# Optimization experiments

Hardware: AMD Instinct MI355X
Metric: run time of the kernel (lower is better)

Reference implementation:

```python
import jax, jax.numpy as jnp
import numpy as np

B, S = 512, 64
ZD, GD, SK = 256, 16, 512   # vel_z_dim, genre_cond_dim, skel_encode_dim
H = 1024                    # vel_hidden_dim
ND, VC = 9, 4               # n_drum_classes, vel_cond_dim


def _gru(x, h, Wi, Wh, bi, bh):
    # torch.nn.GRUCell math; gates ordered [r, z, n]
    gi = x @ Wi.T + bi
    gh = h @ Wh.T + bh
    i_r, i_z, i_n = jnp.split(gi, 3, axis=-1)
    h_r, h_z, h_n = jnp.split(gh, 3, axis=-1)
    r = jax.nn.sigmoid(i_r + h_r)
    zg = jax.nn.sigmoid(i_z + h_z)
    n = jnp.tanh(i_n + r * h_n)
    return (1.0 - zg) * n + zg * h


def setup_inputs() -> dict:
    key = jax.random.key(0)
    ks = jax.random.split(key, 14)
    rn = lambda k, shp, s: jax.random.normal(k, shp, dtype=jnp.float32) * s
    return dict(
        z=rn(ks[0], (B, ZD), 1.0),
        note_encoded=rn(ks[1], (B, SK), 1.0),
        vel_target=jax.random.uniform(ks[2], (B, S, ND), dtype=jnp.float32),
        note=jax.random.uniform(ks[3], (B, S, ND), dtype=jnp.float32),
        vel_cond=jax.random.uniform(ks[4], (B, S, VC), dtype=jnp.float32),
        genre_cond=rn(ks[5], (B, GD), 1.0),
        W_in=rn(ks[6], (H, ZD + SK + GD), 0.02), b_in=jnp.zeros((H,), jnp.float32),
        W_ih1=rn(ks[7], (3 * H, ND * 2 + VC), 0.05), W_hh1=rn(ks[8], (3 * H, H), 0.02),
        b_ih1=jnp.zeros((3 * H,), jnp.float32), b_hh1=jnp.zeros((3 * H,), jnp.float32),
        W_ih2=rn(ks[9], (3 * H, H), 0.02), W_hh2=rn(ks[10], (3 * H, H), 0.02),
        b_ih2=jnp.zeros((3 * H,), jnp.float32), b_hh2=jnp.zeros((3 * H,), jnp.float32),
        W_out=rn(ks[11], (ND, H), 0.02), b_out=jnp.zeros((ND,), jnp.float32),
        training=0, teacher_forcing_ratio=0,
    )


def reference(z, note_encoded, vel_target, note, vel_cond, genre_cond,
              W_in, b_in, W_ih1, W_hh1, b_ih1, b_hh1,
              W_ih2, W_hh2, b_ih2, b_hh2, W_out, b_out,
              training, teacher_forcing_ratio):
    # eval mode: dropout = identity, teacher forcing never taken
    del vel_target, training, teacher_forcing_ratio
    bsz = z.shape[0]
    zc = jnp.concatenate([z.reshape(bsz, -1), note_encoded, genre_cond], axis=-1)
    h1 = jnp.tanh(zc @ W_in.T + b_in)              # [B, H]
    h2 = jnp.zeros_like(h1)                        # overwritten at step 0
    out0 = jnp.zeros((bsz, W_out.shape[0]), z.dtype)

    def step(carry, xs):
        out, h1, h2 = carry
        i, nt, ct = xs
        inp = jnp.concatenate([out, nt, ct], axis=-1)       # [B, 2*ND+VC]
        h1 = _gru(inp, h1, W_ih1, W_hh1, b_ih1, b_hh1)
        h2 = jnp.where(i == 0, h1, h2)                      # hx[1] = hx[0] at i==0
        h2 = _gru(h1, h2, W_ih2, W_hh2, b_ih2, b_hh2)
        vel = jax.nn.sigmoid(h2 @ W_out.T + b_out)          # [B, ND]
        return (vel, h1, h2), vel

    xs = (jnp.arange(note.shape[1]),
          jnp.transpose(note, (1, 0, 2)),
          jnp.transpose(vel_cond, (1, 0, 2)))
    _, outs = jax.lax.scan(step, (out0, h1, h2), xs)
    return jnp.transpose(outs, (1, 0, 2))                    # [B, S, ND]
```

## Files before the change

### kernel.cpp

```cpp
#include <hip/hip_runtime.h>
#include <hip/hip_bf16.h>

#define HD 1024
#define BB 512
#define SS 64
#define N3 3072
#define NC 9216
#define ND 9
#define VC 4

typedef __attribute__((ext_vector_type(8))) short bf16x8;
typedef __attribute__((ext_vector_type(4))) float f32x4;

__device__ __forceinline__ ushort f2b(float f) {
    unsigned u = __builtin_bit_cast(unsigned, f);
    u += 0x7fffu + ((u >> 16) & 1u);
    return (ushort)(u >> 16);
}

__device__ __forceinline__ void gld_lds16(const void* g, void* l) {
    __builtin_amdgcn_global_load_lds(
        (const __attribute__((address_space(1))) unsigned int*)g,
        (__attribute__((address_space(3))) unsigned int*)l, 16, 0, 0);
}

__global__ __launch_bounds__(256) void prep_w(
    const float* __restrict__ Wih2, const float* __restrict__ Whh1,
    const float* __restrict__ Whh2, ushort* __restrict__ Wcat)
{
    const int row = blockIdx.x;
    const float* src = row < 3072 ? Wih2 + (size_t)row * HD
                     : row < 6144 ? Whh1 + (size_t)(row - 3072) * HD
                                  : Whh2 + (size_t)(row - 6144) * HD;
    const int c = threadIdx.x * 4;
    float4 v = *(const float4*)(src + c);
    ushort4 o;
    o.x = f2b(v.x); o.y = f2b(v.y); o.z = f2b(v.z); o.w = f2b(v.w);
    *(ushort4*)(Wcat + (size_t)row * HD + c) = o;
}

__global__ __launch_bounds__(256) void prep_wt1(
    const float* __restrict__ Wih1, float* __restrict__ Wt1)
{
    const int g = blockIdx.x * 256 + threadIdx.x;
    #pragma unroll
    for (int c = 0; c < 22; ++c)
        Wt1[c * N3 + g] = Wih1[(size_t)g * 22 + c];
}

__global__ __launch_bounds__(256) void init_h1(
    const float* __restrict__ z, const float* __restrict__ ne, const float* __restrict__ gc,
    const float* __restrict__ W_in, const float* __restrict__ b_in,
    float* __restrict__ h1, ushort* __restrict__ h1b)
{
    __shared__ float As[16][68];
    __shared__ float Ws[16][68];

    const int tid = threadIdx.x;
    const int bm  = blockIdx.y * 64;
    const int bn  = blockIdx.x * 64;
    const int r   = tid >> 2;
    const int kq  = (tid & 3) << 2;
    const int ty  = tid >> 4;
    const int tx  = tid & 15;
    const int brow = bm + r;

    float acc[4][4] = {};

    for (int k0 = 0; k0 < 784; k0 += 16) {
        const int c = k0 + kq;
        float4 a;
        if (c < 256)      a = *(const float4*)(z  + (size_t)brow * 256 + c);
        else if (c < 768) a = *(const float4*)(ne + (size_t)brow * 512 + (c - 256));
        else              a = *(const float4*)(gc + (size_t)brow * 16  + (c - 768));
        float4 w = *(const float4*)(W_in + (size_t)(bn + r) * 784 + c);
        __syncthreads();
        As[kq+0][r] = a.x; As[kq+1][r] = a.y; As[kq+2][r] = a.z; As[kq+3][r] = a.w;
        Ws[kq+0][r] = w.x; Ws[kq+1][r] = w.y; Ws[kq+2][r] = w.z; Ws[kq+3][r] = w.w;
        __syncthreads();
        #pragma unroll
        for (int k = 0; k < 16; ++k) {
            float4 avv = *(const float4*)&As[k][ty * 4];
            float4 wvv = *(const float4*)&Ws[k][tx * 4];
            const float av[4] = {avv.x, avv.y, avv.z, avv.w};
            const float wv[4] = {wvv.x, wvv.y, wvv.z, wvv.w};
            #pragma unroll
            for (int i = 0; i < 4; ++i)
                #pragma unroll
                for (int j = 0; j < 4; ++j)
                    acc[i][j] = fmaf(av[i], wv[j], acc[i][j]);
        }
    }
    const int col = bn + tx * 4;
    float4 bi = *(const float4*)(b_in + col);
    const float bv[4] = {bi.x, bi.y, bi.z, bi.w};
    #pragma unroll
    for (int i = 0; i < 4; ++i) {
        const int row = bm + ty * 4 + i;
        float4 o = make_float4(tanhf(acc[i][0] + bv[0]), tanhf(acc[i][1] + bv[1]),
                               tanhf(acc[i][2] + bv[2]), tanhf(acc[i][3] + bv[3]));
        *(float4*)(h1 + (size_t)row * HD + col) = o;
        ushort4 ob; ob.x = f2b(o.x); ob.y = f2b(o.y); ob.z = f2b(o.z); ob.w = f2b(o.w);
        *(ushort4*)(h1b + (size_t)row * HD + col) = ob;
    }
}

__global__ __launch_bounds__(256) void gemm3(
    const ushort* __restrict__ h1b, const ushort* __restrict__ h2b,
    const ushort* __restrict__ Wcat, float* __restrict__ Cbuf, int ntb)
{
    __shared__ __align__(16) ushort As[4096];
    __shared__ __align__(16) ushort Ws[4096];

    const int flat = blockIdx.x + (blockIdx.y << 3);
    const int id   = (flat & 7) * gridDim.y + (flat >> 3);
    const int bm   = (id & 7) << 6;
    const int nt   = (id >> 3) + ntb;

    const ushort* Amat = (nt < 96) ? h1b : h2b;
    const ushort* W    = Wcat + (size_t)(nt << 6) * HD;

    const int tid = threadIdx.x;
    const int w   = tid >> 6;
    const int l   = tid & 63;

    const int srow = l >> 3;
    const int sch  = ((l & 7) ^ srow) << 3;
    const ushort* Ag0 = Amat + (size_t)(bm + 16 * w + srow) * HD + sch;
    const ushort* Ag1 = Ag0 + 8 * HD;
    const ushort* Wg0 = W + (size_t)(16 * w + srow) * HD + sch;
    const ushort* Wg1 = Wg0 + 8 * HD;
    ushort* Al0 = As + (16 * w) * 64;
    ushort* Al1 = As + (16 * w + 8) * 64;
    ushort* Wl0 = Ws + (16 * w) * 64;
    ushort* Wl1 = Ws + (16 * w + 8) * 64;

    const int wm = (w >> 1) << 5;
    const int wn = (w & 1) << 5;
    const int fr = l & 15;
    const int fc = l >> 4;

    const int ra0 = wm + fr,  ra1 = wm + 16 + fr;
    const int rb0 = wn + fr,  rb1 = wn + 16 + fr;

    f32x4 acc00 = {0.f,0.f,0.f,0.f}, acc01 = {0.f,0.f,0.f,0.f};
    f32x4 acc10 = {0.f,0.f,0.f,0.f}, acc11 = {0.f,0.f,0.f,0.f};

    for (int kt = 0; kt < 16; ++kt) {
        const int ko = kt << 6;
        __syncthreads();
        gld_lds16(Ag0 + ko, Al0);
        gld_lds16(Ag1 + ko, Al1);
        gld_lds16(Wg0 + ko, Wl0);
        gld_lds16(Wg1 + ko, Wl1);
        __syncthreads();
        #pragma unroll
        for (int kk = 0; kk < 2; ++kk) {
            const int c = (kk << 2) + fc;
            bf16x8 a0 = *(const bf16x8*)(As + ra0 * 64 + ((c ^ (ra0 & 7)) << 3));
            bf16x8 a1 = *(const bf16x8*)(As + ra1 * 64 + ((c ^ (ra1 & 7)) << 3));
            bf16x8 b0 = *(const bf16x8*)(Ws + rb0 * 64 + ((c ^ (rb0 & 7)) << 3));
            bf16x8 b1 = *(const bf16x8*)(Ws + rb1 * 64 + ((c ^ (rb1 & 7)) << 3));
            acc00 = __builtin_amdgcn_mfma_f32_16x16x32_bf16(a0, b0, acc00, 0, 0, 0);
            acc01 = __builtin_amdgcn_mfma_f32_16x16x32_bf16(a0, b1, acc01, 0, 0, 0);
            acc10 = __builtin_amdgcn_mfma_f32_16x16x32_bf16(a1, b0, acc10, 0, 0, 0);
            acc11 = __builtin_amdgcn_mfma_f32_16x16x32_bf16(a1, b1, acc11, 0, 0, 0);
        }
    }

    const int bn = nt << 6;
    float* Cw = Cbuf + (size_t)(bm + wm) * NC + bn + wn;
    #pragma unroll
    for (int r = 0; r < 4; ++r) {
        const size_t ro0 = (size_t)(fc * 4 + r) * NC;
        const size_t ro1 = (size_t)(16 + fc * 4 + r) * NC;
        Cw[ro0 + fr]      = acc00[r];
        Cw[ro0 + 16 + fr] = acc01[r];
        Cw[ro1 + fr]      = acc10[r];
        Cw[ro1 + 16 + fr] = acc11[r];
    }
}

__global__ __launch_bounds__(1024) void gru1_f(
    const float* __restrict__ Cbuf, float* __restrict__ h1, ushort* __restrict__ h1b,
    float* __restrict__ h2, ushort* __restrict__ h2b,
    const float* __restrict__ note, const float* __restrict__ velc,
    const float* __restrict__ dout,
    const float* __restrict__ Wt1, const float* __restrict__ b_ih1,
    const float* __restrict__ b_hh1, int step)
{
    __shared__ float inp[22];
    const int b = blockIdx.x;
    const int j = threadIdx.x;

    if (j < 22) {
        float v;
        if (j < 9)       v = (step == 0) ? 0.f : dout[(size_t)b * (SS * ND) + (step - 1) * ND + j];
        else if (j < 18) v = note[(size_t)b * (SS * ND) + step * ND + (j - 9)];
        else             v = velc[(size_t)b * (SS * VC) + step * VC + (j - 18)];
        inp[j] = v;
    }
    __syncthreads();

    float ir = b_ih1[j], iz = b_ih1[HD + j], inn = b_ih1[2 * HD + j];
    #pragma unroll
    for (int c = 0; c < 22; ++c) {
        const float x = inp[c];
        const float* wr = Wt1 + c * N3;
        ir  = fmaf(x, wr[j],          ir);
        iz  = fmaf(x, wr[HD + j],     iz);
        inn = fmaf(x, wr[2 * HD + j], inn);
    }

    const float* g = Cbuf + (size_t)b * NC + N3;
    const float hr = g[j]          + b_hh1[j];
    const float hz = g[HD + j]     + b_hh1[HD + j];
    const float hn = g[2 * HD + j] + b_hh1[2 * HD + j];

    const float rg = 1.f / (1.f + __expf(-(ir + hr)));
    const float zg = 1.f / (1.f + __expf(-(iz + hz)));
    const float n  = tanhf(inn + rg * hn);
    const float hnew = (1.f - zg) * n + zg * h1[(size_t)b * HD + j];
    h1[(size_t)b * HD + j]  = hnew;
    const ushort hb = f2b(hnew);
    h1b[(size_t)b * HD + j] = hb;
    if (step == 0) {
        h2[(size_t)b * HD + j]  = hnew;
        h2b[(size_t)b * HD + j] = hb;
    }
}

__global__ __launch_bounds__(1024) void gru2_out(
    const float* __restrict__ Cbuf, float* __restrict__ h2, ushort* __restrict__ h2b,
    const float* __restrict__ b_ih2, const float* __restrict__ b_hh2,
    const float* __restrict__ W_out, const float* __restrict__ b_out,
    float* __restrict__ dout, int step)
{
    __shared__ float hs[HD];
    const int b = blockIdx.x;
    const int j = threadIdx.x;

    const float* gi = Cbuf + (size_t)b * NC;
    const float* gh = Cbuf + (size_t)b * NC + 2 * N3;

    const float ir  = gi[j]          + b_ih2[j];
    const float hr  = gh[j]          + b_hh2[j];
    const float iz  = gi[HD + j]     + b_ih2[HD + j];
    const float hz  = gh[HD + j]     + b_hh2[HD + j];
    const float inn = gi[2 * HD + j] + b_ih2[2 * HD + j];
    const float hn  = gh[2 * HD + j] + b_hh2[2 * HD + j];

    const float rg = 1.f / (1.f + __expf(-(ir + hr)));
    const float zg = 1.f / (1.f + __expf(-(iz + hz)));
    const float n  = tanhf(inn + rg * hn);
    const float hnew = (1.f - zg) * n + zg * h2[(size_t)b * HD + j];
    h2[(size_t)b * HD + j]  = hnew;
    h2b[(size_t)b * HD + j] = f2b(hnew);
    hs[j] = hnew;
    __syncthreads();

    const int w = j >> 6;
    const int t = j & 63;
    if (w < ND) {
        float a = 0.f;
        const float* wr = W_out + (size_t)w * HD;
        #pragma unroll
        for (int k = 0; k < HD / 64; ++k)
            a = fmaf(hs[t + k * 64], wr[t + k * 64], a);
        #pragma unroll
        for (int off = 32; off > 0; off >>= 1) a += __shfl_down(a, off);
        if (t == 0)
            dout[(size_t)b * (SS * ND) + step * ND + w] =
                1.f / (1.f + __expf(-(a + b_out[w])));
    }
}

extern "C" void kernel_launch(void* const* d_in, const int* in_sizes, int n_in,
                              void* d_out, int out_size, void* d_ws, size_t ws_size,
                              hipStream_t stream)
{
    const float* z     = (const float*)d_in[0];
    const float* ne    = (const float*)d_in[1];
    const float* note  = (const float*)d_in[3];
    const float* velc  = (const float*)d_in[4];
    const float* gc    = (const float*)d_in[5];
    const float* W_in  = (const float*)d_in[6];
    const float* b_in  = (const float*)d_in[7];
    const float* W_ih1 = (const float*)d_in[8];
    const float* W_hh1 = (const float*)d_in[9];
    const float* b_ih1 = (const float*)d_in[10];
    const float* b_hh1 = (const float*)d_in[11];
    const float* W_ih2 = (const float*)d_in[12];
    const float* W_hh2 = (const float*)d_in[13];
    const float* b_ih2 = (const float*)d_in[14];
    const float* b_hh2 = (const float*)d_in[15];
    const float* W_out = (const float*)d_in[16];
    const float* b_out = (const float*)d_in[17];
    float* out = (float*)d_out;

    float* h1   = (float*)d_ws;
    float* h2   = h1 + BB * HD;
    float* Cbuf = h2 + BB * HD;
    float* Wt1  = Cbuf + (size_t)BB * NC;
    ushort* h1b = (ushort*)(Wt1 + 22 * N3);
    ushort* h2b = h1b + BB * HD;
    ushort* Wcat = h2b + BB * HD;

    prep_w <<<dim3(NC), 256, 0, stream>>>(W_ih2, W_hh1, W_hh2, Wcat);
    prep_wt1<<<dim3(12), 256, 0, stream>>>(W_ih1, Wt1);
    init_h1<<<dim3(16, 8), 256, 0, stream>>>(z, ne, gc, W_in, b_in, h1, h1b);

    gemm3<<<dim3(8, 48), 256, 0, stream>>>(h1b, h2b, Wcat, Cbuf, 48);

    for (int s = 0; s < SS; ++s) {
        gru1_f<<<dim3(BB), 1024, 0, stream>>>(Cbuf, h1, h1b, h2, h2b,
                                              note, velc, out, Wt1, b_ih1, b_hh1, s);
        gemm3<<<dim3(8, 144), 256, 0, stream>>>(h1b, h2b, Wcat, Cbuf, 0);
        gru2_out<<<dim3(BB), 1024, 0, stream>>>(Cbuf, h2, h2b, b_ih2, b_hh2,
                                                W_out, b_out, out, s);
    }
}
```

Before: 2.150 ms.

## Fuse GRU pointwise stages across steps, widen GEMM tile, MFMA init GEMM

Reschedules the recurrence so each step runs one GEMM and one fused pointwise kernel. The fused kernel computes the layer-2 GRU update and the output projection, then the next step's layer-1 GRU update, using the W_hh1·h1 product already held in Cbuf. This removes one launch per step and a round-trip of h1. The shared GEMM now uses 64x128 tiles with 8 MFMAs per k-slice for more reuse, at the cost of fewer blocks. The initial tanh(W_in·zc) becomes a bf16 MFMA GEMM over padded inputs instead of an fp32 SIMT GEMM, which lowers precision for that layer.

```diff
diff --git a/kernel.cpp b/kernel.cpp
--- a/kernel.cpp
+++ b/kernel.cpp
@@ -8,6 +8,7 @@
 #define NC 9216
 #define ND 9
 #define VC 4
+#define KI 832
 
 typedef __attribute__((ext_vector_type(8))) short bf16x8;
 typedef __attribute__((ext_vector_type(4))) float f32x4;
@@ -48,156 +49,235 @@
         Wt1[c * N3 + g] = Wih1[(size_t)g * 22 + c];
 }
 
-__global__ __launch_bounds__(256) void init_h1(
-    const float* __restrict__ z, const float* __restrict__ ne, const float* __restrict__ gc,
-    const float* __restrict__ W_in, const float* __restrict__ b_in,
-    float* __restrict__ h1, ushort* __restrict__ h1b)
-{
-    __shared__ float As[16][68];
-    __shared__ float Ws[16][68];
-
-    const int tid = threadIdx.x;
-    const int bm  = blockIdx.y * 64;
-    const int bn  = blockIdx.x * 64;
-    const int r   = tid >> 2;
-    const int kq  = (tid & 3) << 2;
-    const int ty  = tid >> 4;
-    const int tx  = tid & 15;
-    const int brow = bm + r;
-
-    float acc[4][4] = {};
-
-    for (int k0 = 0; k0 < 784; k0 += 16) {
-        const int c = k0 + kq;
-        float4 a;
-        if (c < 256)      a = *(const float4*)(z  + (size_t)brow * 256 + c);
-        else if (c < 768) a = *(const float4*)(ne + (size_t)brow * 512 + (c - 256));
-        else              a = *(const float4*)(gc + (size_t)brow * 16  + (c - 768));
-        float4 w = *(const float4*)(W_in + (size_t)(bn + r) * 784 + c);
-        __syncthreads();
-        As[kq+0][r] = a.x; As[kq+1][r] = a.y; As[kq+2][r] = a.z; As[kq+3][r] = a.w;
-        Ws[kq+0][r] = w.x; Ws[kq+1][r] = w.y; Ws[kq+2][r] = w.z; Ws[kq+3][r] = w.w;
-        __syncthreads();
-        #pragma unroll
-        for (int k = 0; k < 16; ++k) {
-            float4 avv = *(const float4*)&As[k][ty * 4];
-            float4 wvv = *(const float4*)&Ws[k][tx * 4];
-            const float av[4] = {avv.x, avv.y, avv.z, avv.w};
-            const float wv[4] = {wvv.x, wvv.y, wvv.z, wvv.w};
-            #pragma unroll
-            for (int i = 0; i < 4; ++i)
-                #pragma unroll
-                for (int j = 0; j < 4; ++j)
-                    acc[i][j] = fmaf(av[i], wv[j], acc[i][j]);
-        }
-    }
-    const int col = bn + tx * 4;
-    float4 bi = *(const float4*)(b_in + col);
-    const float bv[4] = {bi.x, bi.y, bi.z, bi.w};
-    #pragma unroll
-    for (int i = 0; i < 4; ++i) {
-        const int row = bm + ty * 4 + i;
-        float4 o = make_float4(tanhf(acc[i][0] + bv[0]), tanhf(acc[i][1] + bv[1]),
-                               tanhf(acc[i][2] + bv[2]), tanhf(acc[i][3] + bv[3]));
-        *(float4*)(h1 + (size_t)row * HD + col) = o;
-        ushort4 ob; ob.x = f2b(o.x); ob.y = f2b(o.y); ob.z = f2b(o.z); ob.w = f2b(o.w);
-        *(ushort4*)(h1b + (size_t)row * HD + col) = ob;
-    }
+__global__ __launch_bounds__(256) void prep_acat(
+    const float* __restrict__ z, const float* __restrict__ ne,
+    const float* __restrict__ gc, ushort* __restrict__ Acat)
+{
+    const int b = blockIdx.x;
+    const int t = threadIdx.x;
+    if (t >= 208) return;
+    const int c = t * 4;
+    float4 v = make_float4(0.f, 0.f, 0.f, 0.f);
+    if (c < 256)      v = *(const float4*)(z  + (size_t)b * 256 + c);
+    else if (c < 768) v = *(const float4*)(ne + (size_t)b * 512 + (c - 256));
+    else if (c < 784) v = *(const float4*)(gc + (size_t)b * 16  + (c - 768));
+    ushort4 o;
+    o.x = f2b(v.x); o.y = f2b(v.y); o.z = f2b(v.z); o.w = f2b(v.w);
+    *(ushort4*)(Acat + (size_t)b * KI + c) = o;
+}
+
+__global__ __launch_bounds__(256) void prep_win(
+    const float* __restrict__ W_in, ushort* __restrict__ W_inb)
+{
+    const int r = blockIdx.x;
+    const int t = threadIdx.x;
+    if (t >= 208) return;
+    const int c = t * 4;
+    ushort4 o = {0, 0, 0, 0};
+    if (c < 784) {
+        float4 v = *(const float4*)(W_in + (size_t)r * 784 + c);
+        o.x = f2b(v.x); o.y = f2b(v.y); o.z = f2b(v.z); o.w = f2b(v.w);
+    }
+    *(ushort4*)(W_inb + (size_t)r * KI + c) = o;
 }
 
 __global__ __launch_bounds__(256) void gemm3(
     const ushort* __restrict__ h1b, const ushort* __restrict__ h2b,
     const ushort* __restrict__ Wcat, float* __restrict__ Cbuf, int ntb)
 {
-    __shared__ __align__(16) ushort As[4096];
-    __shared__ __align__(16) ushort Ws[4096];
+    __shared__ __align__(16) ushort As[64 * 64];
+    __shared__ __align__(16) ushort Bs[128 * 64];
 
     const int flat = blockIdx.x + (blockIdx.y << 3);
     const int id   = (flat & 7) * gridDim.y + (flat >> 3);
-    const int bm   = (id & 7) << 6;
-    const int nt   = (id >> 3) + ntb;
-
-    const ushort* Amat = (nt < 96) ? h1b : h2b;
-    const ushort* W    = Wcat + (size_t)(nt << 6) * HD;
+    const int mt   = id & 7;
+    const int n2   = (id >> 3) + ntb;
+    const int bm   = mt << 6;
+
+    const ushort* Amat = (n2 < 48) ? h1b : h2b;
+    const ushort* Wb   = Wcat + (size_t)(n2 << 7) * HD;
 
     const int tid = threadIdx.x;
     const int w   = tid >> 6;
     const int l   = tid & 63;
-
-    const int srow = l >> 3;
-    const int sch  = ((l & 7) ^ srow) << 3;
-    const ushort* Ag0 = Amat + (size_t)(bm + 16 * w + srow) * HD + sch;
+    const int lr  = l >> 3;
+    const int sw  = ((l & 7) ^ lr) << 3;
+
+    const ushort* Ag0 = Amat + (size_t)(bm + 16 * w + lr) * HD + sw;
     const ushort* Ag1 = Ag0 + 8 * HD;
-    const ushort* Wg0 = W + (size_t)(16 * w + srow) * HD + sch;
-    const ushort* Wg1 = Wg0 + 8 * HD;
+    const ushort* Bg0 = Wb + (size_t)(32 * w + lr) * HD + sw;
+    const ushort* Bg1 = Bg0 + 8 * HD;
+    const ushort* Bg2 = Bg0 + 16 * HD;
+    const ushort* Bg3 = Bg0 + 24 * HD;
     ushort* Al0 = As + (16 * w) * 64;
     ushort* Al1 = As + (16 * w + 8) * 64;
-    ushort* Wl0 = Ws + (16 * w) * 64;
-    ushort* Wl1 = Ws + (16 * w + 8) * 64;
-
-    const int wm = (w >> 1) << 5;
-    const int wn = (w & 1) << 5;
-    const int fr = l & 15;
-    const int fc = l >> 4;
-
-    const int ra0 = wm + fr,  ra1 = wm + 16 + fr;
-    const int rb0 = wn + fr,  rb1 = wn + 16 + fr;
-
-    f32x4 acc00 = {0.f,0.f,0.f,0.f}, acc01 = {0.f,0.f,0.f,0.f};
-    f32x4 acc10 = {0.f,0.f,0.f,0.f}, acc11 = {0.f,0.f,0.f,0.f};
+    ushort* Bl0 = Bs + (32 * w) * 64;
+    ushort* Bl1 = Bs + (32 * w + 8) * 64;
+    ushort* Bl2 = Bs + (32 * w + 16) * 64;
+    ushort* Bl3 = Bs + (32 * w + 24) * 64;
+
+    const int wm2 = w >> 1;
+    const int wn2 = w & 1;
+    const int fr  = l & 15;
+    const int fc  = l >> 4;
+
+    f32x4 acc[2][4] = {};
 
     for (int kt = 0; kt < 16; ++kt) {
         const int ko = kt << 6;
         __syncthreads();
         gld_lds16(Ag0 + ko, Al0);
         gld_lds16(Ag1 + ko, Al1);
-        gld_lds16(Wg0 + ko, Wl0);
-        gld_lds16(Wg1 + ko, Wl1);
+        gld_lds16(Bg0 + ko, Bl0);
+        gld_lds16(Bg1 + ko, Bl1);
+        gld_lds16(Bg2 + ko, Bl2);
+        gld_lds16(Bg3 + ko, Bl3);
         __syncthreads();
         #pragma unroll
         for (int kk = 0; kk < 2; ++kk) {
             const int c = (kk << 2) + fc;
-            bf16x8 a0 = *(const bf16x8*)(As + ra0 * 64 + ((c ^ (ra0 & 7)) << 3));
-            bf16x8 a1 = *(const bf16x8*)(As + ra1 * 64 + ((c ^ (ra1 & 7)) << 3));
-            bf16x8 b0 = *(const bf16x8*)(Ws + rb0 * 64 + ((c ^ (rb0 & 7)) << 3));
-            bf16x8 b1 = *(const bf16x8*)(Ws + rb1 * 64 + ((c ^ (rb1 & 7)) << 3));
-            acc00 = __builtin_amdgcn_mfma_f32_16x16x32_bf16(a0, b0, acc00, 0, 0, 0);
-            acc01 = __builtin_amdgcn_mfma_f32_16x16x32_bf16(a0, b1, acc01, 0, 0, 0);
-            acc10 = __builtin_amdgcn_mfma_f32_16x16x32_bf16(a1, b0, acc10, 0, 0, 0);
-            acc11 = __builtin_amdgcn_mfma_f32_16x16x32_bf16(a1, b1, acc11, 0, 0, 0);
-        }
-    }
-
-    const int bn = nt << 6;
-    float* Cw = Cbuf + (size_t)(bm + wm) * NC + bn + wn;
+            bf16x8 a[2], b[4];
+            #pragma unroll
+            for (int i = 0; i < 2; ++i) {
+                const int ra = (wm2 << 5) + (i << 4) + fr;
+                a[i] = *(const bf16x8*)(As + ra * 64 + ((c ^ (ra & 7)) << 3));
+            }
+            #pragma unroll
+            for (int j = 0; j < 4; ++j) {
+                const int rb = (wn2 << 6) + (j << 4) + fr;
+                b[j] = *(const bf16x8*)(Bs + rb * 64 + ((c ^ (rb & 7)) << 3));
+            }
+            #pragma unroll
+            for (int i = 0; i < 2; ++i)
+                #pragma unroll
+                for (int j = 0; j < 4; ++j)
+                    acc[i][j] = __builtin_amdgcn_mfma_f32_16x16x32_bf16(a[i], b[j], acc[i][j], 0, 0, 0);
+        }
+    }
+
+    const int bn = n2 << 7;
     #pragma unroll
-    for (int r = 0; r < 4; ++r) {
-        const size_t ro0 = (size_t)(fc * 4 + r) * NC;
-        const size_t ro1 = (size_t)(16 + fc * 4 + r) * NC;
-        Cw[ro0 + fr]      = acc00[r];
-        Cw[ro0 + 16 + fr] = acc01[r];
-        Cw[ro1 + fr]      = acc10[r];
-        Cw[ro1 + 16 + fr] = acc11[r];
-    }
-}
-
-__global__ __launch_bounds__(1024) void gru1_f(
+    for (int i = 0; i < 2; ++i) {
+        const int row0 = bm + (wm2 << 5) + (i << 4) + (fc << 2);
+        #pragma unroll
+        for (int r = 0; r < 4; ++r) {
+            float* Crow = Cbuf + (size_t)(row0 + r) * NC + bn + (wn2 << 6) + fr;
+            Crow[0]  = acc[i][0][r];
+            Crow[16] = acc[i][1][r];
+            Crow[32] = acc[i][2][r];
+            Crow[48] = acc[i][3][r];
+        }
+    }
+}
+
+__global__ __launch_bounds__(256) void gemm_init(
+    const ushort* __restrict__ Acat, const ushort* __restrict__ W_inb,
+    const float* __restrict__ b_in, float* __restrict__ h1, ushort* __restrict__ h1b)
+{
+    __shared__ __align__(16) ushort As[64 * 64];
+    __shared__ __align__(16) ushort Bs[128 * 64];
+
+    const int flat = blockIdx.x + (blockIdx.y << 3);
+    const int id   = (flat & 7) * gridDim.y + (flat >> 3);
+    const int mt   = id & 7;
+    const int n2   = id >> 3;
+    const int bm   = mt << 6;
+
+    const ushort* Wb = W_inb + (size_t)(n2 << 7) * KI;
+
+    const int tid = threadIdx.x;
+    const int w   = tid >> 6;
+    const int l   = tid & 63;
+    const int lr  = l >> 3;
+    const int sw  = ((l & 7) ^ lr) << 3;
+
+    const ushort* Ag0 = Acat + (size_t)(bm + 16 * w + lr) * KI + sw;
+    const ushort* Ag1 = Ag0 + 8 * KI;
+    const ushort* Bg0 = Wb + (size_t)(32 * w + lr) * KI + sw;
+    const ushort* Bg1 = Bg0 + 8 * KI;
+    const ushort* Bg2 = Bg0 + 16 * KI;
+    const ushort* Bg3 = Bg0 + 24 * KI;
+    ushort* Al0 = As + (16 * w) * 64;
+    ushort* Al1 = As + (16 * w + 8) * 64;
+    ushort* Bl0 = Bs + (32 * w) * 64;
+    ushort* Bl1 = Bs + (32 * w + 8) * 64;
+    ushort* Bl2 = Bs + (32 * w + 16) * 64;
+    ushort* Bl3 = Bs + (32 * w + 24) * 64;
+
+    const int wm2 = w >> 1;
+    const int wn2 = w & 1;
+    const int fr  = l & 15;
+    const int fc  = l >> 4;
+
+    f32x4 acc[2][4] = {};
+
+    for (int kt = 0; kt < 13; ++kt) {
+        const int ko = kt << 6;
+        __syncthreads();
+        gld_lds16(Ag0 + ko, Al0);
+        gld_lds16(Ag1 + ko, Al1);
+        gld_lds16(Bg0 + ko, Bl0);
+        gld_lds16(Bg1 + ko, Bl1);
+        gld_lds16(Bg2 + ko, Bl2);
+        gld_lds16(Bg3 + ko, Bl3);
+        __syncthreads();
+        #pragma unroll
+        for (int kk = 0; kk < 2; ++kk) {
+            const int c = (kk << 2) + fc;
+            bf16x8 a[2], b[4];
+            #pragma unroll
+            for (int i = 0; i < 2; ++i) {
+                const int ra = (wm2 << 5) + (i << 4) + fr;
+                a[i] = *(const bf16x8*)(As + ra * 64 + ((c ^ (ra & 7)) << 3));
+            }
+            #pragma unroll
+            for (int j = 0; j < 4; ++j) {
+                const int rb = (wn2 << 6) + (j << 4) + fr;
+                b[j] = *(const bf16x8*)(Bs + rb * 64 + ((c ^ (rb & 7)) << 3));
+            }
+            #pragma unroll
+            for (int i = 0; i < 2; ++i)
+                #pragma unroll
+                for (int j = 0; j < 4; ++j)
+                    acc[i][j] = __builtin_amdgcn_mfma_f32_16x16x32_bf16(a[i], b[j], acc[i][j], 0, 0, 0);
+        }
+    }
+
+    const int bn = (n2 << 7) + (wn2 << 6) + fr;
+    float bj[4];
+    #pragma unroll
+    for (int j = 0; j < 4; ++j) bj[j] = b_in[bn + (j << 4)];
+    #pragma unroll
+    for (int i = 0; i < 2; ++i) {
+        const int row0 = bm + (wm2 << 5) + (i << 4) + (fc << 2);
+        #pragma unroll
+        for (int r = 0; r < 4; ++r) {
+            #pragma unroll
+            for (int j = 0; j < 4; ++j) {
+                const float v = tanhf(acc[i][j][r] + bj[j]);
+                const size_t idx = (size_t)(row0 + r) * HD + bn + (j << 4);
+                h1[idx]  = v;
+                h1b[idx] = f2b(v);
+            }
+        }
+    }
+}
+
+__global__ __launch_bounds__(1024) void gru1_first(
     const float* __restrict__ Cbuf, float* __restrict__ h1, ushort* __restrict__ h1b,
     float* __restrict__ h2, ushort* __restrict__ h2b,
     const float* __restrict__ note, const float* __restrict__ velc,
-    const float* __restrict__ dout,
     const float* __restrict__ Wt1, const float* __restrict__ b_ih1,
-    const float* __restrict__ b_hh1, int step)
+    const float* __restrict__ b_hh1)
 {
     __shared__ float inp[22];
     const int b = blockIdx.x;
     const int j = threadIdx.x;
 
     if (j < 22) {
-        float v;
-        if (j < 9)       v = (step == 0) ? 0.f : dout[(size_t)b * (SS * ND) + (step - 1) * ND + j];
-        else if (j < 18) v = note[(size_t)b * (SS * ND) + step * ND + (j - 9)];
-        else             v = velc[(size_t)b * (SS * VC) + step * VC + (j - 18)];
+        float v = 0.f;
+        if (j >= 9 && j < 18) v = note[(size_t)b * (SS * ND) + (j - 9)];
+        else if (j >= 18)     v = velc[(size_t)b * (SS * VC) + (j - 18)];
         inp[j] = v;
     }
     __syncthreads();
@@ -221,27 +301,35 @@
     const float zg = 1.f / (1.f + __expf(-(iz + hz)));
     const float n  = tanhf(inn + rg * hn);
     const float hnew = (1.f - zg) * n + zg * h1[(size_t)b * HD + j];
+    const ushort hb = f2b(hnew);
     h1[(size_t)b * HD + j]  = hnew;
-    const ushort hb = f2b(hnew);
     h1b[(size_t)b * HD + j] = hb;
-    if (step == 0) {
-        h2[(size_t)b * HD + j]  = hnew;
-        h2b[(size_t)b * HD + j] = hb;
-    }
-}
-
-__global__ __launch_bounds__(1024) void gru2_out(
-    const float* __restrict__ Cbuf, float* __restrict__ h2, ushort* __restrict__ h2b,
+    h2[(size_t)b * HD + j]  = hnew;
+    h2b[(size_t)b * HD + j] = hb;
+}
+
+__global__ __launch_bounds__(1024) void pw_fused(
+    const float* __restrict__ Cbuf, float* __restrict__ h1, ushort* __restrict__ h1b,
+    float* __restrict__ h2, ushort* __restrict__ h2b,
+    const float* __restrict__ note, const float* __restrict__ velc,
+    const float* __restrict__ Wt1,
+    const float* __restrict__ b_ih1, const float* __restrict__ b_hh1,
     const float* __restrict__ b_ih2, const float* __restrict__ b_hh2,
     const float* __restrict__ W_out, const float* __restrict__ b_out,
     float* __restrict__ dout, int step)
 {
     __shared__ float hs[HD];
+    __shared__ float inp[22];
     const int b = blockIdx.x;
     const int j = threadIdx.x;
 
+    if (step + 1 < SS && j >= 9 && j < 22) {
+        inp[j] = (j < 18) ? note[(size_t)b * (SS * ND) + (step + 1) * ND + (j - 9)]
+                          : velc[(size_t)b * (SS * VC) + (step + 1) * VC + (j - 18)];
+    }
+
     const float* gi = Cbuf + (size_t)b * NC;
-    const float* gh = Cbuf + (size_t)b * NC + 2 * N3;
+    const float* gh = gi + 2 * N3;
 
     const float ir  = gi[j]          + b_ih2[j];
     const float hr  = gh[j]          + b_hh2[j];
@@ -269,9 +357,35 @@
             a = fmaf(hs[t + k * 64], wr[t + k * 64], a);
         #pragma unroll
         for (int off = 32; off > 0; off >>= 1) a += __shfl_down(a, off);
-        if (t == 0)
-            dout[(size_t)b * (SS * ND) + step * ND + w] =
-                1.f / (1.f + __expf(-(a + b_out[w])));
+        if (t == 0) {
+            const float o = 1.f / (1.f + __expf(-(a + b_out[w])));
+            dout[(size_t)b * (SS * ND) + step * ND + w] = o;
+            inp[w] = o;
+        }
+    }
+    __syncthreads();
+
+    if (step + 1 < SS) {
+        float xir = b_ih1[j], xiz = b_ih1[HD + j], xinn = b_ih1[2 * HD + j];
+        #pragma unroll
+        for (int c = 0; c < 22; ++c) {
+            const float x = inp[c];
+            const float* wr = Wt1 + c * N3;
+            xir  = fmaf(x, wr[j],          xir);
+            xiz  = fmaf(x, wr[HD + j],     xiz);
+            xinn = fmaf(x, wr[2 * HD + j], xinn);
+        }
+        const float* g1 = Cbuf + (size_t)b * NC + N3;
+        const float hr1 = g1[j]          + b_hh1[j];
+        const float hz1 = g1[HD + j]     + b_hh1[HD + j];
+        const float hn1 = g1[2 * HD + j] + b_hh1[2 * HD + j];
+
+        const float rg1 = 1.f / (1.f + __expf(-(xir + hr1)));
+        const float zg1 = 1.f / (1.f + __expf(-(xiz + hz1)));
+        const float n1  = tanhf(xinn + rg1 * hn1);
+        const float h1new = (1.f - zg1) * n1 + zg1 * h1[(size_t)b * HD + j];
+        h1[(size_t)b * HD + j]  = h1new;
+        h1b[(size_t)b * HD + j] = f2b(h1new);
     }
 }
 
@@ -298,25 +412,32 @@
     const float* b_out = (const float*)d_in[17];
     float* out = (float*)d_out;
 
-    float* h1   = (float*)d_ws;
-    float* h2   = h1 + BB * HD;
-    float* Cbuf = h2 + BB * HD;
-    float* Wt1  = Cbuf + (size_t)BB * NC;
-    ushort* h1b = (ushort*)(Wt1 + 22 * N3);
-    ushort* h2b = h1b + BB * HD;
+    float*  h1   = (float*)d_ws;
+    float*  h2   = h1 + BB * HD;
+    float*  Cbuf = h2 + BB * HD;
+    float*  Wt1  = Cbuf + (size_t)BB * NC;
+    ushort* h1b  = (ushort*)(Wt1 + 22 * N3);
+    ushort* h2b  = h1b + BB * HD;
     ushort* Wcat = h2b + BB * HD;
-
-    prep_w <<<dim3(NC), 256, 0, stream>>>(W_ih2, W_hh1, W_hh2, Wcat);
-    prep_wt1<<<dim3(12), 256, 0, stream>>>(W_ih1, Wt1);
-    init_h1<<<dim3(16, 8), 256, 0, stream>>>(z, ne, gc, W_in, b_in, h1, h1b);
-
-    gemm3<<<dim3(8, 48), 256, 0, stream>>>(h1b, h2b, Wcat, Cbuf, 48);
+    ushort* Acat  = (ushort*)Cbuf;
+    ushort* W_inb = Acat + (size_t)BB * KI;
+
+    prep_w   <<<dim3(NC),  256, 0, stream>>>(W_ih2, W_hh1, W_hh2, Wcat);
+    prep_wt1 <<<dim3(12),  256, 0, stream>>>(W_ih1, Wt1);
+    prep_acat<<<dim3(BB),  256, 0, stream>>>(z, ne, gc, Acat);
+    prep_win <<<dim3(HD),  256, 0, stream>>>(W_in, W_inb);
+
+    gemm_init<<<dim3(8, 8), 256, 0, stream>>>(Acat, W_inb, b_in, h1, h1b);
+
+    gemm3<<<dim3(8, 24), 256, 0, stream>>>(h1b, h2b, Wcat, Cbuf, 24);
+    gru1_first<<<dim3(BB), 1024, 0, stream>>>(Cbuf, h1, h1b, h2, h2b,
+                                              note, velc, Wt1, b_ih1, b_hh1);
 
     for (int s = 0; s < SS; ++s) {
-        gru1_f<<<dim3(BB), 1024, 0, stream>>>(Cbuf, h1, h1b, h2, h2b,
-                                              note, velc, out, Wt1, b_ih1, b_hh1, s);
-        gemm3<<<dim3(8, 144), 256, 0, stream>>>(h1b, h2b, Wcat, Cbuf, 0);
-        gru2_out<<<dim3(BB), 1024, 0, stream>>>(Cbuf, h2, h2b, b_ih2, b_hh2,
+        gemm3<<<dim3(8, 72), 256, 0, stream>>>(h1b, h2b, Wcat, Cbuf, 0);
+        pw_fused<<<dim3(BB), 1024, 0, stream>>>(Cbuf, h1, h1b, h2, h2b,
+                                                note, velc, Wt1,
+                                                b_ih1, b_hh1, b_ih2, b_hh2,
                                                 W_out, b_out, out, s);
     }
 }
```

Measured after the change: 2.228 ms. 3.6% more time.

## Fuse next-step GRU1 pointwise into GRU2 kernel and use MFMA for init GEMM

Applied to the files above, without the earlier changes.

Moves the layer-1 GRU pointwise update for step s+1 into the same kernel that computes layer-2 update and output for step s. Step 0's layer-1 update is peeled into a separate kernel. This removes one kernel launch and one global round trip of gate data per timestep. The initial hidden-state projection is also rewritten as a bf16 MFMA GEMM on pre-converted, K-padded inputs, which adds conversion kernels and reduces precision for the initial state.

```diff
diff --git a/kernel.cpp b/kernel.cpp
--- a/kernel.cpp
+++ b/kernel.cpp
@@ -8,6 +8,7 @@
 #define NC 9216
 #define ND 9
 #define VC 4
+#define KI 832
 
 typedef __attribute__((ext_vector_type(8))) short bf16x8;
 typedef __attribute__((ext_vector_type(4))) float f32x4;
@@ -16,6 +17,10 @@
     unsigned u = __builtin_bit_cast(unsigned, f);
     u += 0x7fffu + ((u >> 16) & 1u);
     return (ushort)(u >> 16);
+}
+
+__device__ __forceinline__ float sigf(float x) {
+    return 1.f / (1.f + __expf(-x));
 }
 
 __device__ __forceinline__ void gld_lds16(const void* g, void* l) {
@@ -48,60 +53,107 @@
         Wt1[c * N3 + g] = Wih1[(size_t)g * 22 + c];
 }
 
-__global__ __launch_bounds__(256) void init_h1(
-    const float* __restrict__ z, const float* __restrict__ ne, const float* __restrict__ gc,
-    const float* __restrict__ W_in, const float* __restrict__ b_in,
-    float* __restrict__ h1, ushort* __restrict__ h1b)
-{
-    __shared__ float As[16][68];
-    __shared__ float Ws[16][68];
+__global__ __launch_bounds__(256) void prep_acat(
+    const float* __restrict__ z, const float* __restrict__ ne,
+    const float* __restrict__ gc, ushort* __restrict__ Acat)
+{
+    const int b = blockIdx.x;
+    const int t = threadIdx.x;
+    if (t >= 208) return;
+    const int c = t * 4;
+    float4 v = make_float4(0.f, 0.f, 0.f, 0.f);
+    if (c < 256)      v = *(const float4*)(z  + (size_t)b * 256 + c);
+    else if (c < 768) v = *(const float4*)(ne + (size_t)b * 512 + (c - 256));
+    else if (c < 784) v = *(const float4*)(gc + (size_t)b * 16  + (c - 768));
+    ushort4 o;
+    o.x = f2b(v.x); o.y = f2b(v.y); o.z = f2b(v.z); o.w = f2b(v.w);
+    *(ushort4*)(Acat + (size_t)b * KI + c) = o;
+}
+
+__global__ __launch_bounds__(256) void prep_win(
+    const float* __restrict__ W_in, ushort* __restrict__ W_inb)
+{
+    const int r = blockIdx.x;
+    const int t = threadIdx.x;
+    if (t >= 208) return;
+    const int c = t * 4;
+    ushort4 o = {0, 0, 0, 0};
+    if (c < 784) {
+        float4 v = *(const float4*)(W_in + (size_t)r * 784 + c);
+        o.x = f2b(v.x); o.y = f2b(v.y); o.z = f2b(v.z); o.w = f2b(v.w);
+    }
+    *(ushort4*)(W_inb + (size_t)r * KI + c) = o;
+}
+
+__global__ __launch_bounds__(256) void k_init(
+    const ushort* __restrict__ Acat, const ushort* __restrict__ W_inb,
+    const float* __restrict__ b_in, float* __restrict__ h1, ushort* __restrict__ h1b)
+{
+    __shared__ __align__(16) ushort As[2 * 4096];
+    __shared__ __align__(16) ushort Bs[2 * 4096];
+    const int t = blockIdx.x;
+    const int nt = t >> 3, mt = t & 7;
 
     const int tid = threadIdx.x;
-    const int bm  = blockIdx.y * 64;
-    const int bn  = blockIdx.x * 64;
-    const int r   = tid >> 2;
-    const int kq  = (tid & 3) << 2;
-    const int ty  = tid >> 4;
-    const int tx  = tid & 15;
-    const int brow = bm + r;
-
-    float acc[4][4] = {};
-
-    for (int k0 = 0; k0 < 784; k0 += 16) {
-        const int c = k0 + kq;
-        float4 a;
-        if (c < 256)      a = *(const float4*)(z  + (size_t)brow * 256 + c);
-        else if (c < 768) a = *(const float4*)(ne + (size_t)brow * 512 + (c - 256));
-        else              a = *(const float4*)(gc + (size_t)brow * 16  + (c - 768));
-        float4 w = *(const float4*)(W_in + (size_t)(bn + r) * 784 + c);
+    const int w = tid >> 6, l = tid & 63;
+    const int lr = l >> 3;
+    const int sw = ((l & 7) ^ lr) << 3;
+
+    const ushort* Ag0 = Acat + ((size_t)(mt << 6)) * KI + (size_t)(16 * w + lr) * KI + sw;
+    const ushort* Ag1 = Ag0 + 8 * KI;
+    const ushort* Bg0 = W_inb + ((size_t)(nt << 6)) * KI + (size_t)(16 * w + lr) * KI + sw;
+    const ushort* Bg1 = Bg0 + 8 * KI;
+    const int o0 = (16 * w) * 64, o1 = (16 * w + 8) * 64;
+
+    gld_lds16(Ag0, As + o0); gld_lds16(Ag1, As + o1);
+    gld_lds16(Bg0, Bs + o0); gld_lds16(Bg1, Bs + o1);
+
+    const int wm = (w >> 1) << 5, wn = (w & 1) << 5;
+    const int fr = l & 15, fc = l >> 4;
+    const int ra0 = wm + fr, ra1 = wm + 16 + fr;
+    const int rb0 = wn + fr, rb1 = wn + 16 + fr;
+
+    f32x4 acc[2][2] = {};
+    for (int kt = 0; kt < 13; ++kt) {
+        const int cb = (kt & 1) << 12;
         __syncthreads();
-        As[kq+0][r] = a.x; As[kq+1][r] = a.y; As[kq+2][r] = a.z; As[kq+3][r] = a.w;
-        Ws[kq+0][r] = w.x; Ws[kq+1][r] = w.y; Ws[kq+2][r] = w.z; Ws[kq+3][r] = w.w;
-        __syncthreads();
-        #pragma unroll
-        for (int k = 0; k < 16; ++k) {
-            float4 avv = *(const float4*)&As[k][ty * 4];
-            float4 wvv = *(const float4*)&Ws[k][tx * 4];
-            const float av[4] = {avv.x, avv.y, avv.z, avv.w};
-            const float wv[4] = {wvv.x, wvv.y, wvv.z, wvv.w};
-            #pragma unroll
-            for (int i = 0; i < 4; ++i)
-                #pragma unroll
-                for (int j = 0; j < 4; ++j)
-                    acc[i][j] = fmaf(av[i], wv[j], acc[i][j]);
-        }
-    }
-    const int col = bn + tx * 4;
-    float4 bi = *(const float4*)(b_in + col);
-    const float bv[4] = {bi.x, bi.y, bi.z, bi.w};
+        if (kt + 1 < 13) {
+            const int nb = ((kt + 1) & 1) << 12;
+            const int ko = (kt + 1) << 6;
+            gld_lds16(Ag0 + ko, As + nb + o0);
+            gld_lds16(Ag1 + ko, As + nb + o1);
+            gld_lds16(Bg0 + ko, Bs + nb + o0);
+            gld_lds16(Bg1 + ko, Bs + nb + o1);
+        }
+        #pragma unroll
+        for (int kk = 0; kk < 2; ++kk) {
+            const int c = (kk << 2) + fc;
+            bf16x8 a0 = *(const bf16x8*)(As + cb + ra0 * 64 + ((c ^ (ra0 & 7)) << 3));
+            bf16x8 a1 = *(const bf16x8*)(As + cb + ra1 * 64 + ((c ^ (ra1 & 7)) << 3));
+            bf16x8 b0 = *(const bf16x8*)(Bs + cb + rb0 * 64 + ((c ^ (rb0 & 7)) << 3));
+            bf16x8 b1 = *(const bf16x8*)(Bs + cb + rb1 * 64 + ((c ^ (rb1 & 7)) << 3));
+            acc[0][0] = __builtin_amdgcn_mfma_f32_16x16x32_bf16(a0, b0, acc[0][0], 0, 0, 0);
+            acc[0][1] = __builtin_amdgcn_mfma_f32_16x16x32_bf16(a0, b1, acc[0][1], 0, 0, 0);
+            acc[1][0] = __builtin_amdgcn_mfma_f32_16x16x32_bf16(a1, b0, acc[1][0], 0, 0, 0);
+            acc[1][1] = __builtin_amdgcn_mfma_f32_16x16x32_bf16(a1, b1, acc[1][1], 0, 0, 0);
+        }
+    }
+
+    const int row0 = (mt << 6) + wm;
+    const int col0 = (nt << 6) + wn + fr;
+    const float b0v = b_in[col0], b1v = b_in[col0 + 16];
     #pragma unroll
-    for (int i = 0; i < 4; ++i) {
-        const int row = bm + ty * 4 + i;
-        float4 o = make_float4(tanhf(acc[i][0] + bv[0]), tanhf(acc[i][1] + bv[1]),
-                               tanhf(acc[i][2] + bv[2]), tanhf(acc[i][3] + bv[3]));
-        *(float4*)(h1 + (size_t)row * HD + col) = o;
-        ushort4 ob; ob.x = f2b(o.x); ob.y = f2b(o.y); ob.z = f2b(o.z); ob.w = f2b(o.w);
-        *(ushort4*)(h1b + (size_t)row * HD + col) = ob;
+    for (int i = 0; i < 2; ++i) {
+        #pragma unroll
+        for (int r = 0; r < 4; ++r) {
+            const int row = row0 + i * 16 + fc * 4 + r;
+            const float v0 = tanhf(acc[i][0][r] + b0v);
+            const float v1 = tanhf(acc[i][1][r] + b1v);
+            h1[(size_t)row * HD + col0]       = v0;
+            h1b[(size_t)row * HD + col0]      = f2b(v0);
+            h1[(size_t)row * HD + col0 + 16]  = v1;
+            h1b[(size_t)row * HD + col0 + 16] = f2b(v1);
+        }
     }
 }
 
@@ -181,23 +233,21 @@
     }
 }
 
-__global__ __launch_bounds__(1024) void gru1_f(
+__global__ __launch_bounds__(1024) void gru1_first(
     const float* __restrict__ Cbuf, float* __restrict__ h1, ushort* __restrict__ h1b,
     float* __restrict__ h2, ushort* __restrict__ h2b,
     const float* __restrict__ note, const float* __restrict__ velc,
-    const float* __restrict__ dout,
     const float* __restrict__ Wt1, const float* __restrict__ b_ih1,
-    const float* __restrict__ b_hh1, int step)
+    const float* __restrict__ b_hh1)
 {
     __shared__ float inp[22];
     const int b = blockIdx.x;
     const int j = threadIdx.x;
 
     if (j < 22) {
-        float v;
-        if (j < 9)       v = (step == 0) ? 0.f : dout[(size_t)b * (SS * ND) + (step - 1) * ND + j];
-        else if (j < 18) v = note[(size_t)b * (SS * ND) + step * ND + (j - 9)];
-        else             v = velc[(size_t)b * (SS * VC) + step * VC + (j - 18)];
+        float v = 0.f;
+        if (j >= 9 && j < 18) v = note[(size_t)b * (SS * ND) + (j - 9)];
+        else if (j >= 18)     v = velc[(size_t)b * (SS * VC) + (j - 18)];
         inp[j] = v;
     }
     __syncthreads();
@@ -217,31 +267,39 @@
     const float hz = g[HD + j]     + b_hh1[HD + j];
     const float hn = g[2 * HD + j] + b_hh1[2 * HD + j];
 
-    const float rg = 1.f / (1.f + __expf(-(ir + hr)));
-    const float zg = 1.f / (1.f + __expf(-(iz + hz)));
+    const float rg = sigf(ir + hr);
+    const float zg = sigf(iz + hz);
     const float n  = tanhf(inn + rg * hn);
     const float hnew = (1.f - zg) * n + zg * h1[(size_t)b * HD + j];
+    const ushort hb = f2b(hnew);
     h1[(size_t)b * HD + j]  = hnew;
-    const ushort hb = f2b(hnew);
     h1b[(size_t)b * HD + j] = hb;
-    if (step == 0) {
-        h2[(size_t)b * HD + j]  = hnew;
-        h2b[(size_t)b * HD + j] = hb;
-    }
-}
-
-__global__ __launch_bounds__(1024) void gru2_out(
-    const float* __restrict__ Cbuf, float* __restrict__ h2, ushort* __restrict__ h2b,
+    h2[(size_t)b * HD + j]  = hnew;
+    h2b[(size_t)b * HD + j] = hb;
+}
+
+__global__ __launch_bounds__(1024) void pw_fused(
+    const float* __restrict__ Cbuf, float* __restrict__ h1, ushort* __restrict__ h1b,
+    float* __restrict__ h2, ushort* __restrict__ h2b,
+    const float* __restrict__ note, const float* __restrict__ velc,
+    const float* __restrict__ Wt1,
+    const float* __restrict__ b_ih1, const float* __restrict__ b_hh1,
     const float* __restrict__ b_ih2, const float* __restrict__ b_hh2,
     const float* __restrict__ W_out, const float* __restrict__ b_out,
     float* __restrict__ dout, int step)
 {
     __shared__ float hs[HD];
+    __shared__ float inp[22];
     const int b = blockIdx.x;
     const int j = threadIdx.x;
 
+    if (step + 1 < SS && j >= 9 && j < 22) {
+        inp[j] = (j < 18) ? note[(size_t)b * (SS * ND) + (step + 1) * ND + (j - 9)]
+                          : velc[(size_t)b * (SS * VC) + (step + 1) * VC + (j - 18)];
+    }
+
     const float* gi = Cbuf + (size_t)b * NC;
-    const float* gh = Cbuf + (size_t)b * NC + 2 * N3;
+    const float* gh = gi + 2 * N3;
 
     const float ir  = gi[j]          + b_ih2[j];
     const float hr  = gh[j]          + b_hh2[j];
@@ -250,8 +308,8 @@
     const float inn = gi[2 * HD + j] + b_ih2[2 * HD + j];
     const float hn  = gh[2 * HD + j] + b_hh2[2 * HD + j];
 
-    const float rg = 1.f / (1.f + __expf(-(ir + hr)));
-    const float zg = 1.f / (1.f + __expf(-(iz + hz)));
+    const float rg = sigf(ir + hr);
+    const float zg = sigf(iz + hz);
     const float n  = tanhf(inn + rg * hn);
     const float hnew = (1.f - zg) * n + zg * h2[(size_t)b * HD + j];
     h2[(size_t)b * HD + j]  = hnew;
@@ -269,9 +327,35 @@
             a = fmaf(hs[t + k * 64], wr[t + k * 64], a);
         #pragma unroll
         for (int off = 32; off > 0; off >>= 1) a += __shfl_down(a, off);
-        if (t == 0)
-            dout[(size_t)b * (SS * ND) + step * ND + w] =
-                1.f / (1.f + __expf(-(a + b_out[w])));
+        if (t == 0) {
+            const float o = sigf(a + b_out[w]);
+            dout[(size_t)b * (SS * ND) + step * ND + w] = o;
+            inp[w] = o;
+        }
+    }
+    __syncthreads();
+
+    if (step + 1 < SS) {
+        float xir = b_ih1[j], xiz = b_ih1[HD + j], xinn = b_ih1[2 * HD + j];
+        #pragma unroll
+        for (int c = 0; c < 22; ++c) {
+            const float x = inp[c];
+            const float* wr = Wt1 + c * N3;
+            xir  = fmaf(x, wr[j],          xir);
+            xiz  = fmaf(x, wr[HD + j],     xiz);
+            xinn = fmaf(x, wr[2 * HD + j], xinn);
+        }
+        const float* g1 = Cbuf + (size_t)b * NC + N3;
+        const float hr1 = g1[j]          + b_hh1[j];
+        const float hz1 = g1[HD + j]     + b_hh1[HD + j];
+        const float hn1 = g1[2 * HD + j] + b_hh1[2 * HD + j];
+
+        const float rg1 = sigf(xir + hr1);
+        const float zg1 = sigf(xiz + hz1);
+        const float n1  = tanhf(xinn + rg1 * hn1);
+        const float h1new = (1.f - zg1) * n1 + zg1 * h1[(size_t)b * HD + j];
+        h1[(size_t)b * HD + j]  = h1new;
+        h1b[(size_t)b * HD + j] = f2b(h1new);
     }
 }
 
@@ -298,25 +382,32 @@
     const float* b_out = (const float*)d_in[17];
     float* out = (float*)d_out;
 
-    float* h1   = (float*)d_ws;
-    float* h2   = h1 + BB * HD;
-    float* Cbuf = h2 + BB * HD;
-    float* Wt1  = Cbuf + (size_t)BB * NC;
-    ushort* h1b = (ushort*)(Wt1 + 22 * N3);
-    ushort* h2b = h1b + BB * HD;
+    float*  h1   = (float*)d_ws;
+    float*  h2   = h1 + BB * HD;
+    float*  Cbuf = h2 + BB * HD;
+    float*  Wt1  = Cbuf + (size_t)BB * NC;
+    ushort* h1b  = (ushort*)(Wt1 + 22 * N3);
+    ushort* h2b  = h1b + BB * HD;
     ushort* Wcat = h2b + BB * HD;
-
-    prep_w <<<dim3(NC), 256, 0, stream>>>(W_ih2, W_hh1, W_hh2, Wcat);
-    prep_wt1<<<dim3(12), 256, 0, stream>>>(W_ih1, Wt1);
-    init_h1<<<dim3(16, 8), 256, 0, stream>>>(z, ne, gc, W_in, b_in, h1, h1b);
+    ushort* Acat  = (ushort*)Cbuf;
+    ushort* W_inb = Acat + (size_t)BB * KI;
+
+    prep_w   <<<dim3(NC), 256, 0, stream>>>(W_ih2, W_hh1, W_hh2, Wcat);
+    prep_wt1 <<<dim3(12), 256, 0, stream>>>(W_ih1, Wt1);
+    prep_acat<<<dim3(BB), 256, 0, stream>>>(z, ne, gc, Acat);
+    prep_win <<<dim3(HD), 256, 0, stream>>>(W_in, W_inb);
+
+    k_init<<<dim3(128), 256, 0, stream>>>(Acat, W_inb, b_in, h1, h1b);
 
     gemm3<<<dim3(8, 48), 256, 0, stream>>>(h1b, h2b, Wcat, Cbuf, 48);
+    gru1_first<<<dim3(BB), 1024, 0, stream>>>(Cbuf, h1, h1b, h2, h2b,
+                                              note, velc, Wt1, b_ih1, b_hh1);
 
     for (int s = 0; s < SS; ++s) {
-        gru1_f<<<dim3(BB), 1024, 0, stream>>>(Cbuf, h1, h1b, h2, h2b,
-                                              note, velc, out, Wt1, b_ih1, b_hh1, s);
         gemm3<<<dim3(8, 144), 256, 0, stream>>>(h1b, h2b, Wcat, Cbuf, 0);
-        gru2_out<<<dim3(BB), 1024, 0, stream>>>(Cbuf, h2, h2b, b_ih2, b_hh2,
+        pw_fused<<<dim3(BB), 1024, 0, stream>>>(Cbuf, h1, h1b, h2, h2b,
+                                                note, velc, Wt1,
+                                                b_ih1, b_hh1, b_ih2, b_hh2,
                                                 W_out, b_out, out, s);
     }
 }
```

Measured after the change: 2.094 ms. 1.03x faster.
